# Performance work log

Hardware: AMD Instinct MI355X
Metric: run time of the kernel (lower is better)

Reference implementation:

```python
import jax, jax.numpy as jnp
import numpy as np

N = 50000      # nodes
E = 800000     # edges
IN_DIM = 256
D = 32         # out_dim per head
H = 8          # num_heads
NEG_SLOPE = 0.01  # torch F.leaky_relu default


def setup_inputs() -> dict:
    key = jax.random.key(0)
    k1, k2, k3, k4, k5 = jax.random.split(key, 5)
    h = jax.random.normal(k1, (N, IN_DIM), dtype=jnp.float32)
    W = jax.random.normal(k2, (H, IN_DIM, D), dtype=jnp.float32) * 0.05
    attn_w = jax.random.normal(k3, (H, 2 * D), dtype=jnp.float32) * 0.05
    src = jax.random.randint(k4, (E,), 0, N, dtype=jnp.int64)
    dst = jax.random.randint(k5, (E,), 0, N, dtype=jnp.int64)
    return {"h": h, "W": W, "attn_w": attn_w, "src": src, "dst": dst}


def reference(h, W, attn_w, src, dst):
    # per-head linear projection: z[n,h,d]
    z = jnp.einsum('ni,hid->nhd', h, W)
    # attn_fc(concat(z_src, z_dst)) = z_src @ a_l + z_dst @ a_r
    a_l, a_r = attn_w[:, :D], attn_w[:, D:]
    el = jnp.einsum('nhd,hd->nh', z, a_l)  # [N,H]
    er = jnp.einsum('nhd,hd->nh', z, a_r)  # [N,H]
    e = jax.nn.leaky_relu(el[src] + er[dst], NEG_SLOPE)  # [E,H]
    # segment softmax over incoming edges of each destination node
    m = jax.ops.segment_max(e, dst, num_segments=N)      # [N,H]
    m = jnp.where(jnp.isfinite(m), m, 0.0)               # nodes w/ no in-edges
    num = jnp.exp(e - m[dst])                            # [E,H]
    den = jax.ops.segment_sum(num, dst, num_segments=N)  # [N,H]
    den_e = den[dst]
    alpha = num / jnp.where(den_e > 0, den_e, 1.0)       # [E,H]
    # weighted scatter-sum of source features
    msg = alpha[:, :, None] * z[src]                     # [E,H,D]
    hout = jax.ops.segment_sum(msg, dst, num_segments=N) # [N,H,D]
    # merge='cat': concat head outputs along feature dim
    return hout.reshape(N, H * D)
```

## Files before the change

kernel.cpp:

```cpp
#include <hip/hip_runtime.h>
#include <hip/hip_bf16.h>
#include <math.h>

#define NN 50000
#define EE 800000
#define INDIM 256
#define DD 32
#define HH 8
#define CC 256
#define NEG 0.01f
#define NREP 8
#define NSCAN 49
#define PREP_GRID 2048
#define PREP_STRIDE (PREP_GRID * 256)

typedef __attribute__((ext_vector_type(8))) short bf16x8;
typedef __attribute__((ext_vector_type(4))) float f32x4;

__device__ __forceinline__ unsigned short f32_to_bf16_rne(float f) {
  unsigned u = __float_as_uint(f);
  u += 0x7fffu + ((u >> 16) & 1u);
  return (unsigned short)(u >> 16);
}
__device__ __forceinline__ unsigned pack_bf16x2(float a, float b) {
  __hip_bfloat162 p = __float22bfloat162_rn(make_float2(a, b));
  return *reinterpret_cast<unsigned*>(&p);
}

__global__ __launch_bounds__(256) void k_prep(const unsigned* __restrict__ sraw,
                                              const unsigned* __restrict__ draw,
                                              int* __restrict__ counts8,
                                              unsigned* __restrict__ sd32,
                                              unsigned short* __restrict__ slot16,
                                              const float* __restrict__ W,
                                              unsigned short* __restrict__ WbT) {
  __shared__ int sflag;
  if (threadIdx.x == 0) sflag = 0;
  __syncthreads();
  const int gt = blockIdx.x * 256 + threadIdx.x;
  unsigned v = 0;
#pragma unroll
  for (int i = 0; i < 2; ++i) {
    int e = (gt * 2 + i) % (EE / 2);
    v |= sraw[2 * e + 1] | draw[2 * e + 1];
  }
  if (v) atomicOr(&sflag, 1);
  __syncthreads();
  const int is32 = sflag;

  const int rep = blockIdx.x & (NREP - 1);
  int* __restrict__ mycounts = counts8 + rep * NN;

  for (int e = gt; e < EE; e += PREP_STRIDE) {
    int sv, dv;
    if (is32) {
      sv = ((const int*)sraw)[e];
      dv = ((const int*)draw)[e];
    } else {
      sv = (int)((const long long*)sraw)[e];
      dv = (int)((const long long*)draw)[e];
    }
    sd32[e] = ((unsigned)dv << 16) | (unsigned)sv;
    slot16[e] = (unsigned short)atomicAdd(&mycounts[dv], 1);
  }

  if (gt < INDIM * CC) {
    int n = gt >> 8, k = gt & 255;
    int hh = n >> 5, d = n & 31;
    WbT[gt] = f32_to_bf16_rne(W[(size_t)hh * 8192 + k * 32 + d]);
  }
}

__global__ __launch_bounds__(512) void k_gemm(const float* __restrict__ h,
                                              const unsigned short* __restrict__ WbT,
                                              const float* __restrict__ attn_w,
                                              signed char* __restrict__ z8,
                                              float* __restrict__ elsc,
                                              float* __restrict__ er) {
  __shared__ short sA[64 * 256];
  const int t = threadIdx.x;
  const int l = t & 63;
  const int w = t >> 6;
  const int row0 = blockIdx.x * 64;

#pragma unroll
  for (int i = 0; i < 4; ++i) {
    int q = i * 512 + t;
    int row = q >> 5, c = q & 31;
    int grow = row0 + row; if (grow >= NN) grow = NN - 1;
    const float* src = &h[(size_t)grow * 256 + c * 8];
    float4 f0 = *reinterpret_cast<const float4*>(src);
    float4 f1 = *reinterpret_cast<const float4*>(src + 4);
    uint4 pk;
    pk.x = pack_bf16x2(f0.x, f0.y);
    pk.y = pack_bf16x2(f0.z, f0.w);
    pk.z = pack_bf16x2(f1.x, f1.y);
    pk.w = pack_bf16x2(f1.z, f1.w);
    int sc = c ^ (row & 7);
    *reinterpret_cast<uint4*>(&sA[row * 256 + sc * 8]) = pk;
  }

  bf16x8 bf[2][8];
  {
    const int n = w * 32 + (l & 15);
    const int kb = (l >> 4) * 8;
#pragma unroll
    for (int c = 0; c < 2; ++c)
#pragma unroll
      for (int kk = 0; kk < 8; ++kk)
        bf[c][kk] = *reinterpret_cast<const bf16x8*>(
            &WbT[(size_t)(n + c * 16) * 256 + kk * 32 + kb]);
  }

  f32x4 acc[4][2];
#pragma unroll
  for (int m = 0; m < 4; ++m)
#pragma unroll
    for (int c = 0; c < 2; ++c) acc[m][c] = (f32x4){0.f, 0.f, 0.f, 0.f};

  __syncthreads();

#pragma unroll
  for (int kk = 0; kk < 8; ++kk) {
    bf16x8 af[4];
#pragma unroll
    for (int m = 0; m < 4; ++m) {
      int row = m * 16 + (l & 15);
      int chunk = kk * 4 + (l >> 4);
      int sc = chunk ^ (row & 7);
      af[m] = *reinterpret_cast<const bf16x8*>(&sA[row * 256 + sc * 8]);
    }
#pragma unroll
    for (int m = 0; m < 4; ++m)
#pragma unroll
      for (int c = 0; c < 2; ++c)
        acc[m][c] = __builtin_amdgcn_mfma_f32_16x16x32_bf16(bf[c][kk], af[m], acc[m][c], 0, 0, 0);
  }

  float alc[2][4], arc[2][4];
#pragma unroll
  for (int c = 0; c < 2; ++c)
#pragma unroll
    for (int r = 0; r < 4; ++r) {
      int d = c * 16 + ((l >> 4) << 2) + r;
      alc[c][r] = attn_w[w * 64 + d];
      arc[c][r] = attn_w[w * 64 + 32 + d];
    }

#pragma unroll
  for (int m = 0; m < 4; ++m) {
    int node = row0 + m * 16 + (l & 15);
    float pl = 0.f, pr = 0.f, pm = 0.f;
#pragma unroll
    for (int c = 0; c < 2; ++c)
#pragma unroll
      for (int r = 0; r < 4; ++r) {
        float a = acc[m][c][r];
        pl += a * alc[c][r];
        pr += a * arc[c][r];
        pm = fmaxf(pm, fabsf(a));
      }
    pl += __shfl_xor(pl, 16); pl += __shfl_xor(pl, 32);
    pr += __shfl_xor(pr, 16); pr += __shfl_xor(pr, 32);
    pm = fmaxf(pm, __shfl_xor(pm, 16)); pm = fmaxf(pm, __shfl_xor(pm, 32));
    const float rcp = (pm > 0.f) ? (127.f / pm) : 0.f;

    if (node < NN) {
#pragma unroll
      for (int c = 0; c < 2; ++c) {
        unsigned wq = 0;
#pragma unroll
        for (int r = 0; r < 4; ++r) {
          int q = __float2int_rn(acc[m][c][r] * rcp);
          wq |= ((unsigned)(q & 255)) << (8 * r);
        }
        *reinterpret_cast<unsigned*>(
            &z8[(size_t)node * CC + w * 32 + c * 16 + ((l >> 4) << 2)]) = wq;
      }
      if ((l >> 4) == 0) {
        elsc[(size_t)node * 16 + w] = pl;
        elsc[(size_t)node * 16 + 8 + w] = pm * (1.f / 127.f);
        er[(size_t)node * HH + w] = pr;
      }
    }
  }
}

__global__ __launch_bounds__(1024) void k_scan(const int* __restrict__ counts8,
                                               int* __restrict__ row_start,
                                               int* __restrict__ partial,
                                               unsigned char* __restrict__ offs8) {
  __shared__ int s[1024];
  const int tid = threadIdx.x;
  const int i = blockIdx.x * 1024 + tid;
  int deg = 0;
  if (i < NN) {
    unsigned pack0 = 0, pack1 = 0;
    int run = 0;
#pragma unroll
    for (int r = 0; r < NREP; ++r) {
      int c = counts8[r * NN + i];
      if (r < 4) pack0 |= (unsigned)run << (8 * r);
      else       pack1 |= (unsigned)run << (8 * (r - 4));
      run += c;
    }
    deg = run;
    uint2 pk; pk.x = pack0; pk.y = pack1;
    *reinterpret_cast<uint2*>(&offs8[(size_t)i * 8]) = pk;
  }
  s[tid] = deg;
  __syncthreads();
  for (int off = 1; off < 1024; off <<= 1) {
    int tv = (tid >= off) ? s[tid - off] : 0;
    __syncthreads();
    s[tid] += tv;
    __syncthreads();
  }
  if (i < NN) row_start[i] = s[tid] - deg;
  if (tid == 1023) partial[blockIdx.x] = s[1023];
}

__device__ __forceinline__ void block_base_scan(const int* __restrict__ partial,
                                                int* __restrict__ sbase) {
  if (threadIdx.x < 64) {
    int l = threadIdx.x;
    int x = (l < NSCAN) ? partial[l] : 0;
    int orig = x;
#pragma unroll
    for (int off = 1; off < 64; off <<= 1) {
      int y = __shfl_up(x, off);
      if (l >= off) x += y;
    }
    sbase[l] = x - orig;
  }
  __syncthreads();
}

__global__ __launch_bounds__(256) void k_scatter(const unsigned* __restrict__ sd32,
                                                 const unsigned short* __restrict__ slot16,
                                                 const unsigned char* __restrict__ offs8,
                                                 const int* __restrict__ row_start,
                                                 const int* __restrict__ partial,
                                                 unsigned short* __restrict__ csr16) {
  __shared__ int sbase[64];
  block_base_scan(partial, sbase);
  int stride = gridDim.x * blockDim.x;
  for (int e = blockIdx.x * blockDim.x + threadIdx.x; e < EE; e += stride) {
    unsigned sd = sd32[e];
    int dn = (int)(sd >> 16);
    int rep = ((e & (PREP_STRIDE - 1)) >> 8) & (NREP - 1);
    int pos = row_start[dn] + sbase[dn >> 10] + (int)offs8[dn * 8 + rep] + (int)slot16[e];
    csr16[pos] = (unsigned short)(sd & 0xFFFFu);
  }
}

#define AGG_WAVES 8192
__global__ __launch_bounds__(256) void k_agg(const signed char* __restrict__ z8,
                                             const float* __restrict__ elsc,
                                             const float* __restrict__ er,
                                             const int* __restrict__ row_start,
                                             const int* __restrict__ partial,
                                             const unsigned short* __restrict__ csr16,
                                             float* __restrict__ out) {
  __shared__ int sbase[64];
  block_base_scan(partial, sbase);

  const int gw = blockIdx.x * 4 + (threadIdx.x >> 6);
  const int l = threadIdx.x & 63;
  const int head = l >> 3;

  for (int n = gw; n < NN; n += AGG_WAVES) {
    const int beg = row_start[n] + sbase[n >> 10];
    const int end = (n == NN - 1) ? EE : (row_start[n + 1] + sbase[(n + 1) >> 10]);
    const float ern = er[(size_t)n * HH + head];

    float den = 0.f;
    float a0 = 0.f, a1 = 0.f, a2 = 0.f, a3 = 0.f;
#pragma unroll 4
    for (int p = beg; p < end; ++p) {
      int s = (int)csr16[p];
      float v = elsc[(size_t)s * 16 + head] + ern;
      v = (v > 0.f) ? v : v * NEG;
      float wgt = __expf(v);
      float sc = elsc[(size_t)s * 16 + 8 + head];
      unsigned wq = *reinterpret_cast<const unsigned*>(&z8[(size_t)s * CC + 4 * l]);
      den += wgt;
      float ws = wgt * sc;
      a0 += ws * (float)(int)(signed char)(wq & 255);
      a1 += ws * (float)(int)(signed char)((wq >> 8) & 255);
      a2 += ws * (float)(int)(signed char)((wq >> 16) & 255);
      a3 += ws * (float)(int)(signed char)(wq >> 24);
    }
    const float rd = (end > beg) ? (1.f / den) : 0.f;
    float4 o;
    o.x = a0 * rd; o.y = a1 * rd; o.z = a2 * rd; o.w = a3 * rd;
    *reinterpret_cast<float4*>(&out[(size_t)n * CC + 4 * l]) = o;
  }
}

extern "C" void kernel_launch(void* const* d_in, const int* in_sizes, int n_in,
                              void* d_out, int out_size, void* d_ws, size_t ws_size,
                              hipStream_t stream) {
  const float* h      = (const float*)d_in[0];
  const float* W      = (const float*)d_in[1];
  const float* attn_w = (const float*)d_in[2];
  const void*  src_raw = d_in[3];
  const void*  dst_raw = d_in[4];
  float* out = (float*)d_out;

  char* ws = (char*)d_ws;
  size_t off = 0;
  signed char* z8     = (signed char*)(ws + off); off += (size_t)NN * CC;
  unsigned short* WbT = (unsigned short*)(ws + off); off += (size_t)INDIM * CC * 2;
  float* elsc = (float*)(ws + off); off += (size_t)NN * 16 * 4;
  float* er   = (float*)(ws + off); off += (size_t)NN * HH * 4;
  int* counts8 = (int*)(ws + off); off += (size_t)NREP * NN * 4;
  int* row_start = (int*)(ws + off); off += (size_t)NN * 4;
  int* partial   = (int*)(ws + off); off += 256;
  unsigned char* offs8 = (unsigned char*)(ws + off); off += (size_t)NN * 8;
  unsigned* sd32         = (unsigned*)(ws + off); off += (size_t)EE * 4;
  unsigned short* slot16 = (unsigned short*)(ws + off); off += (size_t)EE * 2;
  unsigned short* csr16  = (unsigned short*)(ws + off); off += (size_t)EE * 2;

  hipMemsetAsync(counts8, 0, (size_t)NREP * NN * 4, stream);

  k_prep<<<PREP_GRID, 256, 0, stream>>>((const unsigned*)src_raw, (const unsigned*)dst_raw,
                                        counts8, sd32, slot16, W, WbT);

  k_gemm<<<(NN + 63) / 64, 512, 0, stream>>>(h, WbT, attn_w, z8, elsc, er);

  k_scan<<<NSCAN, 1024, 0, stream>>>(counts8, row_start, partial, offs8);

  k_scatter<<<2048, 256, 0, stream>>>(sd32, slot16, offs8, row_start, partial, csr16);

  k_agg<<<AGG_WAVES / 4, 256, 0, stream>>>(z8, elsc, er, row_start, partial, csr16, out);
}
```

Baseline: 144.2 us.

## Fold degree scan into GEMM launch as extra blocks; double agg waves

Removes the separate k_scan launch by appending 49 extra blocks to the GEMM grid. Each extra block scans 1024 nodes using 512 threads handling two nodes each, storing the scan in the GEMM's shared buffer. This saves one kernel launch and lets the scan run alongside the GEMM. The aggregation kernel's wave count is also doubled, which adds parallelism per node loop but launches more blocks that each redo the base scan.

```diff
diff --git a/kernel.cpp b/kernel.cpp
--- a/kernel.cpp
+++ b/kernel.cpp
@@ -13,6 +13,7 @@
 #define NSCAN 49
 #define PREP_GRID 2048
 #define PREP_STRIDE (PREP_GRID * 256)
+#define GEMM_BLOCKS 782
 
 typedef __attribute__((ext_vector_type(8))) short bf16x8;
 typedef __attribute__((ext_vector_type(4))) float f32x4;
@@ -76,8 +77,53 @@
                                               const float* __restrict__ attn_w,
                                               signed char* __restrict__ z8,
                                               float* __restrict__ elsc,
-                                              float* __restrict__ er) {
+                                              float* __restrict__ er,
+                                              const int* __restrict__ counts8,
+                                              int* __restrict__ row_start,
+                                              int* __restrict__ partial,
+                                              unsigned char* __restrict__ offs8) {
   __shared__ short sA[64 * 256];
+
+  if (blockIdx.x >= GEMM_BLOCKS) {
+    int* si = (int*)sA;
+    const int cb = blockIdx.x - GEMM_BLOCKS;
+    const int tid = threadIdx.x;
+    const int i0 = cb * 1024 + tid * 2;
+    int d0 = 0, d1 = 0;
+#pragma unroll
+    for (int which = 0; which < 2; ++which) {
+      int i = i0 + which;
+      if (i < NN) {
+        unsigned pack0 = 0, pack1 = 0;
+        int run = 0;
+#pragma unroll
+        for (int r = 0; r < NREP; ++r) {
+          int c = counts8[r * NN + i];
+          if (r < 4) pack0 |= (unsigned)run << (8 * r);
+          else       pack1 |= (unsigned)run << (8 * (r - 4));
+          run += c;
+        }
+        if (which == 0) d0 = run; else d1 = run;
+        uint2 pk; pk.x = pack0; pk.y = pack1;
+        *reinterpret_cast<uint2*>(&offs8[(size_t)i * 8]) = pk;
+      }
+    }
+    int pair = d0 + d1;
+    si[tid] = pair;
+    __syncthreads();
+    for (int off = 1; off < 512; off <<= 1) {
+      int tv = (tid >= off) ? si[tid - off] : 0;
+      __syncthreads();
+      si[tid] += tv;
+      __syncthreads();
+    }
+    int ex = si[tid] - pair;
+    if (i0 < NN) row_start[i0] = ex;
+    if (i0 + 1 < NN) row_start[i0 + 1] = ex + d0;
+    if (tid == 511) partial[cb] = si[511];
+    return;
+  }
+
   const int t = threadIdx.x;
   const int l = t & 63;
   const int w = t >> 6;
@@ -184,40 +230,6 @@
       }
     }
   }
-}
-
-__global__ __launch_bounds__(1024) void k_scan(const int* __restrict__ counts8,
-                                               int* __restrict__ row_start,
-                                               int* __restrict__ partial,
-                                               unsigned char* __restrict__ offs8) {
-  __shared__ int s[1024];
-  const int tid = threadIdx.x;
-  const int i = blockIdx.x * 1024 + tid;
-  int deg = 0;
-  if (i < NN) {
-    unsigned pack0 = 0, pack1 = 0;
-    int run = 0;
-#pragma unroll
-    for (int r = 0; r < NREP; ++r) {
-      int c = counts8[r * NN + i];
-      if (r < 4) pack0 |= (unsigned)run << (8 * r);
-      else       pack1 |= (unsigned)run << (8 * (r - 4));
-      run += c;
-    }
-    deg = run;
-    uint2 pk; pk.x = pack0; pk.y = pack1;
-    *reinterpret_cast<uint2*>(&offs8[(size_t)i * 8]) = pk;
-  }
-  s[tid] = deg;
-  __syncthreads();
-  for (int off = 1; off < 1024; off <<= 1) {
-    int tv = (tid >= off) ? s[tid - off] : 0;
-    __syncthreads();
-    s[tid] += tv;
-    __syncthreads();
-  }
-  if (i < NN) row_start[i] = s[tid] - deg;
-  if (tid == 1023) partial[blockIdx.x] = s[1023];
 }
 
 __device__ __forceinline__ void block_base_scan(const int* __restrict__ partial,
@@ -254,7 +266,7 @@
   }
 }
 
-#define AGG_WAVES 8192
+#define AGG_WAVES 16384
 __global__ __launch_bounds__(256) void k_agg(const signed char* __restrict__ z8,
                                              const float* __restrict__ elsc,
                                              const float* __restrict__ er,
@@ -327,9 +339,8 @@
   k_prep<<<PREP_GRID, 256, 0, stream>>>((const unsigned*)src_raw, (const unsigned*)dst_raw,
                                         counts8, sd32, slot16, W, WbT);
 
-  k_gemm<<<(NN + 63) / 64, 512, 0, stream>>>(h, WbT, attn_w, z8, elsc, er);
-
-  k_scan<<<NSCAN, 1024, 0, stream>>>(counts8, row_start, partial, offs8);
+  k_gemm<<<GEMM_BLOCKS + NSCAN, 512, 0, stream>>>(h, WbT, attn_w, z8, elsc, er,
+                                                  counts8, row_start, partial, offs8);
 
   k_scatter<<<2048, 256, 0, stream>>>(sd32, slot16, offs8, row_start, partial, csr16);
 
```

Result: no change. 142.5 us (-1.2%).
